# Kernel optimization log

Measured on AMD Instinct MI355X. Metric: run time of the kernel, lower is better.

## Reference

```python
import jax, jax.numpy as jnp
import numpy as np
from math import sqrt

D_MODEL, N_H, D_H, D_CQ, D_CKV, D_HR = 2048, 16, 128, 768, 512, 64
B, S = 1, 2048


def _rope_cos_sin(seq_len, dim, base=10000.0):
    inv_freq = 1.0 / (base ** (jnp.arange(0, dim, 2, dtype=jnp.float32) / dim))
    ang = jnp.arange(seq_len, dtype=jnp.float32)[:, None] * inv_freq[None, :]  # (S, dim//2)
    return jnp.cos(ang), jnp.sin(ang)


def _rope(t, cos, sin):
    # t: (B, S, ..., dim) with sequence on axis 1; interleaved complex pairs
    shp = t.shape
    d2 = shp[-1] // 2
    tr = t.reshape(shp[:-1] + (d2, 2))
    x0, x1 = tr[..., 0], tr[..., 1]
    bshape = (1, shp[1]) + (1,) * (x0.ndim - 3) + (d2,)
    cs, sn = cos.reshape(bshape), sin.reshape(bshape)
    return jnp.stack([x0 * cs - x1 * sn, x0 * sn + x1 * cs], axis=-1).reshape(shp)


def setup_inputs() -> dict:
    key = jax.random.key(0)
    ks = jax.random.split(key, 10)
    sc = 0.02
    inp = {
        "x": jax.random.normal(ks[0], (B, S, D_MODEL), jnp.float32),
        "mask": jnp.triu(jnp.ones((S, S), dtype=bool), k=1),  # True -> masked (causal)
        "w_norm": jnp.ones((D_MODEL,), jnp.float32),
        "w_cq": jax.random.normal(ks[1], (D_MODEL, D_CQ), jnp.float32) * sc,
        "w_q": jax.random.normal(ks[2], (D_CQ, N_H * D_H), jnp.float32) * sc,
        "w_qr": jax.random.normal(ks[3], (D_CQ, N_H * D_HR), jnp.float32) * sc,
        "w_ckv": jax.random.normal(ks[4], (D_MODEL, D_CKV), jnp.float32) * sc,
        "w_k": jax.random.normal(ks[5], (D_CKV, N_H * D_H), jnp.float32) * sc,
        "w_kr": jax.random.normal(ks[6], (D_MODEL, D_HR), jnp.float32) * sc,
        "w_v": jax.random.normal(ks[7], (D_CKV, D_MODEL), jnp.float32) * sc,
        "w_o": jax.random.normal(ks[8], (N_H * D_H, D_MODEL), jnp.float32) * sc,
    }
    return inp


def reference(x, mask, w_norm, w_cq, w_q, w_qr, w_ckv, w_k, w_kr, w_v, w_o):
    b, s, _ = x.shape
    eps = jnp.finfo(x.dtype).eps
    h = x * jax.lax.rsqrt(jnp.mean(x * x, axis=-1, keepdims=True) + eps) * w_norm  # RMSNorm
    cos, sin = _rope_cos_sin(s, D_HR)

    c_q = h @ w_cq  # (b, s, d_c_q)
    q_c = (c_q @ w_q).reshape(b, s, N_H, D_H).transpose(0, 2, 1, 3)          # (b, h, s, d_h)
    q_r = _rope((c_q @ w_qr).reshape(b, s, N_H, D_HR), cos, sin).transpose(0, 2, 1, 3)
    q = jnp.concatenate([q_c, q_r], axis=-1)  # (b, h, s, d_h + d_h_R)

    c_kv = h @ w_ckv  # (b, s, d_c_kv)
    k_c = (c_kv @ w_k).reshape(b, s, N_H, D_H).transpose(0, 2, 1, 3)
    k_r = _rope(h @ w_kr, cos, sin)[:, None]  # (b, 1, s, d_h_R), shared across heads
    k = jnp.concatenate([k_c, jnp.broadcast_to(k_r, (b, N_H, s, D_HR))], axis=-1)
    v = (c_kv @ w_v).reshape(b, s, N_H, D_H).transpose(0, 2, 1, 3)

    score = jnp.einsum('bhqd,bhkd->bhqk', q, k) / sqrt(D_H + D_HR)
    score = jnp.where(mask, -jnp.inf, score)
    attn = jax.nn.softmax(score, axis=-1)
    out = jnp.einsum('bhqk,bhkd->bhqd', attn, v)  # (b, h, s, d_h)
    out = out.transpose(0, 2, 1, 3).reshape(b, s, N_H * D_H) @ w_o
    return x + out
```

## Files before the change

kernel.cpp:

```cpp
#include <hip/hip_runtime.h>
#include <hip/hip_bf16.h>
#include <math.h>

#define D_MODEL 2048
#define N_H     16
#define D_H     128
#define D_CQ    768
#define D_CKV   512
#define D_HR    64
#define SEQ     2048
#define N_ACT1  1408
#define NSPLIT  4

typedef short bf16x8 __attribute__((ext_vector_type(8)));
typedef float f32x4  __attribute__((ext_vector_type(4)));

__device__ inline short f2bf(float f) {
  union { float f; unsigned u; } v; v.f = f;
  unsigned r = (v.u + 0x7fff + ((v.u >> 16) & 1)) >> 16;
  return (short)r;
}
__device__ inline float bf2f(short s) {
  union { float f; unsigned u; } v; v.u = ((unsigned)(unsigned short)s) << 16;
  return v.f;
}

__device__ inline void gld_lds16(const void* g, void* l) {
#if __has_builtin(__builtin_amdgcn_global_load_lds)
  __builtin_amdgcn_global_load_lds(
      (const __attribute__((address_space(1))) unsigned int*)g,
      (__attribute__((address_space(3))) unsigned int*)l, 16, 0, 0);
#else
  int lane = threadIdx.x & 63;
  *((uint4*)l + lane) = *(const uint4*)g;
#endif
}

struct CastJobs {
  const float* src[8];
  short* dst[8];
  int K[8];
  int pref[9];
  int nx[8];
};

__global__ __launch_bounds__(256) void prep_all(
    CastJobs J, const float* __restrict__ x, const float* __restrict__ wn,
    short* __restrict__ hb) {
  int bid = blockIdx.x;
  int tid = threadIdx.x;

  if (bid >= J.pref[8]) {
    int row = bid - J.pref[8];
    const float* xr = x + (size_t)row * D_MODEL;
    float ss = 0.f;
    for (int i = tid; i < D_MODEL; i += 256) { float v = xr[i]; ss += v * v; }
    __shared__ float red[256];
    red[tid] = ss;
    __syncthreads();
    for (int s = 128; s > 0; s >>= 1) {
      if (tid < s) red[tid] += red[tid + s];
      __syncthreads();
    }
    float scale = rsqrtf(red[0] / (float)D_MODEL + 1.1920929e-7f);
    short* hbr = hb + (size_t)row * D_MODEL;
    for (int i = tid; i < D_MODEL; i += 256) hbr[i] = f2bf(xr[i] * scale * wn[i]);
    return;
  }

  int j = 0;
#pragma unroll
  for (int t = 0; t < 8; t++)
    if (bid >= J.pref[t + 1]) j = t + 1;
  int lid = bid - J.pref[j];
  int nx = J.nx[j];
  int ty = lid / nx, tx = lid - ty * nx;
  int n0 = tx * 64, k0 = ty * 64;
  int K = J.K[j];
  const float* W = J.src[j];
  short* Wt = J.dst[j];
  int Nfull = nx * 64;

  __shared__ short T[64][68];
#pragma unroll
  for (int it = 0; it < 16; it++) {
    int idx = it * 256 + tid;
    int r = idx >> 6, c = idx & 63;
    T[c][r] = f2bf(W[(size_t)(k0 + r) * Nfull + n0 + c]);
  }
  __syncthreads();
#pragma unroll
  for (int it = 0; it < 16; it++) {
    int idx = it * 256 + tid;
    int r = idx >> 6, c = idx & 63;
    Wt[(size_t)(n0 + r) * K + k0 + c] = T[r][c];
  }
}

__device__ __forceinline__ void gemm64_body(
    const short* __restrict__ A, const short* __restrict__ Bt,
    float* __restrict__ Cf, short* __restrict__ Cb, short* __restrict__ Cb2,
    const float* __restrict__ addv, int M, int N, int K, int lda, int ldb,
    int mode, int bxx, int byy) {
  __shared__ short As[2 * 64 * 64];
  __shared__ short Bs[2 * 128 * 64];
  int tid = threadIdx.x;
  int w = tid >> 6, l = tid & 63;
  int lq = l >> 4, l16 = l & 15;
  int bm = byy * 64, bn = bxx * 128;
  int wr = w >> 1, wc = w & 1;
  int wm0 = wr * 32, wn0 = wc * 64;

  f32x4 acc[2][4];
#pragma unroll
  for (int i = 0; i < 2; i++)
#pragma unroll
    for (int j = 0; j < 4; j++) acc[i][j] = (f32x4)0.f;

  int rsub = (l >> 3);
  int csub = ((l & 7) ^ rsub) << 3;

  auto stage = [&](int buf, int k0) {
    short* Asb = As + buf * (64 * 64);
    short* Bsb = Bs + buf * (128 * 64);
#pragma unroll
    for (int i = 0; i < 2; i++) {
      int r0 = i * 32 + w * 8;
      gld_lds16(A + (size_t)(bm + r0 + rsub) * lda + k0 + csub, Asb + r0 * 64);
    }
#pragma unroll
    for (int i = 0; i < 4; i++) {
      int r0 = i * 32 + w * 8;
      gld_lds16(Bt + (size_t)(bn + r0 + rsub) * ldb + k0 + csub, Bsb + r0 * 64);
    }
  };

  stage(0, 0);
  int cur = 0;
  for (int k0 = 0; k0 < K; k0 += 64) {
    __syncthreads();
    if (k0 + 64 < K) stage(cur ^ 1, k0 + 64);
    const short* Asb = As + cur * (64 * 64);
    const short* Bsb = Bs + cur * (128 * 64);

#pragma unroll
    for (int ks = 0; ks < 2; ks++) {
      bf16x8 af[2], bfr[4];
      int sw = ((ks * 4 + lq) ^ (l16 & 7)) << 3;
#pragma unroll
      for (int mt = 0; mt < 2; mt++)
        af[mt] = *(const bf16x8*)&Asb[(wm0 + mt * 16 + l16) * 64 + sw];
#pragma unroll
      for (int nt = 0; nt < 4; nt++)
        bfr[nt] = *(const bf16x8*)&Bsb[(wn0 + nt * 16 + l16) * 64 + sw];
#pragma unroll
      for (int mt = 0; mt < 2; mt++)
#pragma unroll
        for (int nt = 0; nt < 4; nt++)
          acc[mt][nt] = __builtin_amdgcn_mfma_f32_16x16x32_bf16(af[mt], bfr[nt], acc[mt][nt], 0, 0, 0);
    }
    cur ^= 1;
  }

#pragma unroll
  for (int mt = 0; mt < 2; mt++)
#pragma unroll
    for (int i = 0; i < 4; i++) {
      int row = bm + wm0 + mt * 16 + lq * 4 + i;
#pragma unroll
      for (int nt = 0; nt < 4; nt++) {
        int col = bn + wn0 + nt * 16 + l16;
        float v = acc[mt][nt][i];
        if (mode == 0) {
          size_t off = (size_t)row * N + col;
          if (addv) v += addv[off];
          Cf[off] = v;
        } else if (mode == 1) {
          Cb[(size_t)row * N + col] = f2bf(v);
        } else if (mode == 3) {
          if (col < 2048) {
            Cb[((size_t)(col >> 7) * M + row) * 192 + (col & 127)] = f2bf(v);
          } else {
            int cc = col - 2048;
            int hh = cc >> 6, dd = cc & 63;
            float partner = __shfl_xor(v, 1);
            float inv = __expf(-((float)(dd & ~1) / 64.0f) * 9.210340372f);
            float ang = (float)row * inv;
            float c = __cosf(ang), s = __sinf(ang);
            float res = ((dd & 1) == 0) ? (v * c - partner * s)
                                        : (partner * s + v * c);
            Cb[((size_t)hh * M + row) * 192 + 128 + dd] = f2bf(res);
          }
        } else {
          if (col < 2048) {
            Cb[((size_t)(col >> 7) * M + row) * 192 + (col & 127)] = f2bf(v);
          } else {
            Cb2[(size_t)row * D_MODEL + (col - 2048)] = f2bf(v);
          }
        }
      }
    }
}

__global__ __launch_bounds__(256) void gemm_bf16_64(
    const short* __restrict__ A, const short* __restrict__ Bt,
    float* __restrict__ Cf, short* __restrict__ Cb, short* __restrict__ Cb2,
    const float* __restrict__ addv, int M, int N, int K, int lda, int ldb,
    int mode) {
  gemm64_body(A, Bt, Cf, Cb, Cb2, addv, M, N, K, lda, ldb, mode,
              blockIdx.x, blockIdx.y);
}

__global__ __launch_bounds__(256) void gemm_qkv(
    const short* __restrict__ act1, const short* __restrict__ WT2,
    const short* __restrict__ WT3, short* __restrict__ qb,
    short* __restrict__ kb, short* __restrict__ vb) {
  int bx = blockIdx.x;
  if (bx < 24) {
    gemm64_body(act1, WT2, nullptr, qb, nullptr, nullptr,
                SEQ, 3072, D_CQ, N_ACT1, D_CQ, 3, bx, blockIdx.y);
  } else {
    gemm64_body(act1 + 768, WT3, nullptr, kb, vb, nullptr,
                SEQ, 4096, D_CKV, N_ACT1, D_CKV, 4, bx - 24, blockIdx.y);
  }
}

__global__ __launch_bounds__(256) void gemm_fin_split(
    const short* __restrict__ A, const short* __restrict__ Bt,
    float* __restrict__ P) {
  int z = blockIdx.z;
  gemm64_body(A + z * 1024, Bt + z * 1024, P + (size_t)z * SEQ * D_MODEL,
              nullptr, nullptr, nullptr, SEQ, D_MODEL, 1024, D_MODEL, D_MODEL,
              0, blockIdx.x, blockIdx.y);
}

__global__ __launch_bounds__(256) void gemm_fin_merge(
    const float* __restrict__ P, const float* __restrict__ x,
    float* __restrict__ out) {
  size_t i = ((size_t)blockIdx.x * 256 + threadIdx.x) * 4;
  float4 a = *(const float4*)(P + i);
  float4 b = *(const float4*)(P + (size_t)SEQ * D_MODEL + i);
  float4 c = *(const float4*)(x + i);
  float4 o;
  o.x = a.x + b.x + c.x;
  o.y = a.y + b.y + c.y;
  o.z = a.z + b.z + c.z;
  o.w = a.w + b.w + c.w;
  *(float4*)(out + i) = o;
}

__global__ void rope_k_kernel(const short* __restrict__ act1, short* __restrict__ kb) {
  int idx = blockIdx.x * blockDim.x + threadIdx.x;
  if (idx >= SEQ * 32) return;
  int j = idx & 31;
  int s = idx >> 5;
  const short* p = act1 + (size_t)s * N_ACT1 + 1280 + 2 * j;
  float x0 = bf2f(p[0]), x1 = bf2f(p[1]);
  float inv = __expf(-((float)(2 * j) / 64.0f) * 9.210340372f);
  float ang = (float)s * inv;
  float c = __cosf(ang), sn = __sinf(ang);
  short b0 = f2bf(x0 * c - x1 * sn);
  short b1 = f2bf(x0 * sn + x1 * c);
#pragma unroll
  for (int hh = 0; hh < N_H; hh++) {
    short* k = kb + ((size_t)hh * SEQ + s) * 192 + 128 + 2 * j;
    k[0] = b0;
    k[1] = b1;
  }
}

__global__ __launch_bounds__(256) void cast_v_t(
    const short* __restrict__ vb, short* __restrict__ vt) {
  int s0 = blockIdx.x * 64;
  int h = blockIdx.y;
  __shared__ short T[128][72];
  int tid = threadIdx.x;
#pragma unroll
  for (int it = 0; it < 32; it++) {
    int c = it * 256 + tid;
    int r = c >> 7, d = c & 127;
    T[d][r] = vb[(size_t)(s0 + r) * D_MODEL + h * 128 + d];
  }
  __syncthreads();
#pragma unroll
  for (int it = 0; it < 32; it++) {
    int c = it * 256 + tid;
    int d = c >> 6, s = c & 63;
    vt[(size_t)(h * 128 + d) * SEQ + s0 + s] = T[d][s];
  }
}

#define TQ 128
#define TK 64

__global__ __launch_bounds__(256, 2) void attn_mfma(
    const short* __restrict__ qb, const short* __restrict__ kb,
    const short* __restrict__ vt, short* __restrict__ Opart,
    float* __restrict__ Lpart) {
  int bid = blockIdx.x;
  int h = bid & 15;
  int rest = bid >> 4;
  int qt = 15 - (rest / NSPLIT);
  int split = rest % NSPLIT;
  int q0 = qt * TQ;
  int nk = 2 * (qt + 1);
  int tid = threadIdx.x;
  int wave = tid >> 6, lane = tid & 63;
  int lq = lane >> 4, l16 = lane & 15;

  __shared__ short Ks[TK * 192];
  __shared__ short Vs[128 * 64];
  __shared__ short Ps[TQ * 64];

  bf16x8 qf[2][6];
  {
    const short* qp = qb + ((size_t)h * SEQ + q0 + wave * 32 + l16) * 192;
#pragma unroll
    for (int mt = 0; mt < 2; mt++)
#pragma unroll
      for (int ks = 0; ks < 6; ks++)
        qf[mt][ks] = *(const bf16x8*)(qp + (size_t)mt * 16 * 192 + ks * 32 + lq * 8);
  }

  bf16x8 ones;
#pragma unroll
  for (int i = 0; i < 8; i++) ones[i] = (short)0x3F80;

  f32x4 O[2][8];
  f32x4 Ol[2];
#pragma unroll
  for (int mt = 0; mt < 2; mt++) {
    Ol[mt] = (f32x4)0.f;
#pragma unroll
    for (int i = 0; i < 8; i++) O[mt][i] = (f32x4)0.f;
  }
  const float scale = 0.07216878364870323f;

  int goffK[6];
#pragma unroll
  for (int i = 0; i < 6; i++) {
    int s = i * 256 + tid;
    int r = s / 24;
    int c = s - r * 24;
    goffK[i] = r * 192 + ((c ^ (r & 7)) << 3);
  }
  int goffV[4];
  int vrow[4];
#pragma unroll
  for (int i = 0; i < 4; i++) {
    int s = i * 256 + tid;
    int d = s >> 3;
    int p = s & 7;
    vrow[i] = d;
    goffV[i] = (p ^ (d & 7)) << 3;
  }
  const short* kb_h = kb + (size_t)h * SEQ * 192;
  const short* vt_h = vt + (size_t)h * 128 * SEQ;

  auto stage_k = [&](int k0s) {
#pragma unroll
    for (int i = 0; i < 6; i++)
      gld_lds16(kb_h + (size_t)k0s * 192 + goffK[i],
                Ks + (size_t)(i * 256 + wave * 64) * 8);
  };
  auto stage_v = [&](int k0s) {
#pragma unroll
    for (int i = 0; i < 4; i++)
      gld_lds16(vt_h + (size_t)vrow[i] * SEQ + k0s + goffV[i],
                Vs + (size_t)(i * 256 + wave * 64) * 8);
  };

  if (split < nk) stage_k(split * TK);

  for (int t = split; t < nk; t += NSPLIT) {
    int k0 = t * TK;
    __syncthreads();

    stage_v(k0);

    f32x4 S[2][4];
#pragma unroll
    for (int mt = 0; mt < 2; mt++)
#pragma unroll
      for (int nt = 0; nt < 4; nt++) S[mt][nt] = (f32x4)0.f;
    __builtin_amdgcn_s_setprio(1);
#pragma unroll
    for (int ks = 0; ks < 6; ks++) {
#pragma unroll
      for (int nt = 0; nt < 4; nt++) {
        int row = nt * 16 + l16;
        bf16x8 b = *(const bf16x8*)&Ks[row * 192 +
                                       (((ks * 4 + lq) ^ (l16 & 7)) << 3)];
#pragma unroll
        for (int mt = 0; mt < 2; mt++)
          S[mt][nt] = __builtin_amdgcn_mfma_f32_16x16x32_bf16(qf[mt][ks], b, S[mt][nt], 0, 0, 0);
      }
    }
    __builtin_amdgcn_s_setprio(0);

#pragma unroll
    for (int mt = 0; mt < 2; mt++)
#pragma unroll
      for (int i = 0; i < 4; i++) {
        int pr = wave * 32 + mt * 16 + lq * 4 + i;
        int row = q0 + pr;
        bool may = (k0 + 63 > row);
#pragma unroll
        for (int nt = 0; nt < 4; nt++) {
          float p;
          if (may && (k0 + nt * 16 + l16 > row)) p = 0.f;
          else p = __expf(S[mt][nt][i] * scale);
          int j = nt * 16 + l16;
          Ps[pr * 64 + ((((j >> 3) ^ (pr & 7)) << 3) | (j & 7))] = f2bf(p);
        }
      }

    __syncthreads();

    if (t + NSPLIT < nk) stage_k((t + NSPLIT) * TK);

    __builtin_amdgcn_s_setprio(1);
#pragma unroll
    for (int kh = 0; kh < 2; kh++) {
      bf16x8 a[2];
#pragma unroll
      for (int mt = 0; mt < 2; mt++) {
        int prw = wave * 32 + mt * 16 + l16;
        a[mt] = *(const bf16x8*)&Ps[prw * 64 +
                                    (((kh * 4 + lq) ^ (l16 & 7)) << 3)];
        Ol[mt] = __builtin_amdgcn_mfma_f32_16x16x32_bf16(a[mt], ones, Ol[mt], 0, 0, 0);
      }
#pragma unroll
      for (int nt = 0; nt < 8; nt++) {
        int d = nt * 16 + l16;
        bf16x8 b = *(const bf16x8*)&Vs[d * 64 +
                                       (((kh * 4 + lq) ^ (d & 7)) << 3)];
#pragma unroll
        for (int mt = 0; mt < 2; mt++)
          O[mt][nt] = __builtin_amdgcn_mfma_f32_16x16x32_bf16(a[mt], b, O[mt][nt], 0, 0, 0);
      }
    }
    __builtin_amdgcn_s_setprio(0);
  }

#pragma unroll
  for (int mt = 0; mt < 2; mt++)
#pragma unroll
    for (int i = 0; i < 4; i++) {
      int row = q0 + wave * 32 + mt * 16 + lq * 4 + i;
      size_t base = ((size_t)(split * N_H + h) * SEQ + row);
      size_t obase = base * 128;
#pragma unroll
      for (int nt = 0; nt < 8; nt++)
        Opart[obase + nt * 16 + l16] = f2bf(O[mt][nt][i]);
      if (l16 == 0) Lpart[base] = Ol[mt][i];
    }
}

__global__ __launch_bounds__(256) void attn_merge(
    const short* __restrict__ Opart, const float* __restrict__ Lpart,
    short* __restrict__ aob) {
  int q0 = blockIdx.x * 16;
  int h = blockIdx.y;
  int tid = threadIdx.x;
#pragma unroll
  for (int i = 0; i < 8; i++) {
    int c = i * 256 + tid;
    int row = q0 + (c >> 7), d = c & 127;
    float denom = 0.f, num = 0.f;
#pragma unroll
    for (int p = 0; p < NSPLIT; p++) {
      size_t base = (size_t)(p * N_H + h) * SEQ + row;
      denom += Lpart[base];
      num += bf2f(Opart[base * 128 + d]);
    }
    aob[(size_t)row * D_MODEL + h * 128 + d] = f2bf(num / denom);
  }
}

extern "C" void kernel_launch(void* const* d_in, const int* in_sizes, int n_in,
                              void* d_out, int out_size, void* d_ws, size_t ws_size,
                              hipStream_t stream) {
  const float* x      = (const float*)d_in[0];
  const float* w_norm = (const float*)d_in[2];
  const float* w_cq   = (const float*)d_in[3];
  const float* w_q    = (const float*)d_in[4];
  const float* w_qr   = (const float*)d_in[5];
  const float* w_ckv  = (const float*)d_in[6];
  const float* w_k    = (const float*)d_in[7];
  const float* w_kr   = (const float*)d_in[8];
  const float* w_v    = (const float*)d_in[9];
  const float* w_o    = (const float*)d_in[10];
  float* out = (float*)d_out;

  char* ws = (char*)d_ws;
  short* h_bf  = (short*)ws;  ws += (size_t)SEQ * D_MODEL * 2;
  short* act1  = (short*)ws;  ws += (size_t)SEQ * N_ACT1 * 2;
  short* qb    = (short*)ws;  ws += (size_t)N_H * SEQ * 192 * 2;
  short* kb    = (short*)ws;  ws += (size_t)N_H * SEQ * 192 * 2;
  short* vb    = (short*)ws;  ws += (size_t)SEQ * D_MODEL * 2;
  short* vt    = (short*)ws;  ws += (size_t)SEQ * D_MODEL * 2;
  short* ao_bf = (short*)ws;  ws += (size_t)SEQ * D_MODEL * 2;
  short* Opart = (short*)ws;  ws += (size_t)NSPLIT * N_H * SEQ * 128 * 2;
  float* Lpart = (float*)ws;  ws += (size_t)NSPLIT * N_H * SEQ * 4;
  short* WT1   = (short*)ws;  ws += (size_t)N_ACT1 * D_MODEL * 2;
  short* WT2   = (short*)ws;  ws += (size_t)3072 * D_CQ * 2;
  short* WT3   = (short*)ws;  ws += (size_t)4096 * D_CKV * 2;
  short* WTO   = (short*)ws;  ws += (size_t)D_MODEL * D_MODEL * 2;

  float* Pfin = (float*)Opart;

  CastJobs J;
  J.src[0] = w_cq;  J.dst[0] = WT1;                              J.K[0] = D_MODEL; J.nx[0] = D_CQ / 64;
  J.src[1] = w_ckv; J.dst[1] = WT1 + (size_t)768 * D_MODEL;      J.K[1] = D_MODEL; J.nx[1] = D_CKV / 64;
  J.src[2] = w_kr;  J.dst[2] = WT1 + (size_t)1280 * D_MODEL;     J.K[2] = D_MODEL; J.nx[2] = D_HR / 64;
  J.src[3] = w_q;   J.dst[3] = WT2;                              J.K[3] = D_CQ;    J.nx[3] = 2048 / 64;
  J.src[4] = w_qr;  J.dst[4] = WT2 + (size_t)2048 * D_CQ;        J.K[4] = D_CQ;    J.nx[4] = 1024 / 64;
  J.src[5] = w_k;   J.dst[5] = WT3;                              J.K[5] = D_CKV;   J.nx[5] = 2048 / 64;
  J.src[6] = w_v;   J.dst[6] = WT3 + (size_t)2048 * D_CKV;       J.K[6] = D_CKV;   J.nx[6] = 2048 / 64;
  J.src[7] = w_o;   J.dst[7] = WTO;                              J.K[7] = D_MODEL; J.nx[7] = 2048 / 64;
  int pref = 0;
  for (int j = 0; j < 8; j++) {
    J.pref[j] = pref;
    pref += J.nx[j] * (J.K[j] / 64);
  }
  J.pref[8] = pref;
  prep_all<<<pref + SEQ, 256, 0, stream>>>(J, x, w_norm, h_bf);

  gemm_bf16_64<<<dim3(N_ACT1 / 128, SEQ / 64), 256, 0, stream>>>(
      h_bf, WT1, nullptr, act1, nullptr, nullptr, SEQ, N_ACT1, D_MODEL,
      D_MODEL, D_MODEL, 1);

  rope_k_kernel<<<(SEQ * 32 + 255) / 256, 256, 0, stream>>>(act1, kb);

  gemm_qkv<<<dim3(24 + 32, SEQ / 64), 256, 0, stream>>>(
      act1, WT2, WT3, qb, kb, vb);

  cast_v_t<<<dim3(SEQ / 64, N_H), 256, 0, stream>>>(vb, vt);

  attn_mfma<<<dim3((SEQ / TQ) * NSPLIT * N_H), 256, 0, stream>>>(qb, kb, vt, Opart, Lpart);
  attn_merge<<<dim3(SEQ / 16, N_H), 256, 0, stream>>>(Opart, Lpart, ao_bf);

  gemm_fin_split<<<dim3(D_MODEL / 128, SEQ / 64, 2), 256, 0, stream>>>(
      ao_bf, WTO, Pfin);
  gemm_fin_merge<<<(SEQ * D_MODEL) / (256 * 4), 256, 0, stream>>>(
      Pfin, x, out);
}
```

Measured before the change: 306.1 us.

## Fuse V transpose into QKV GEMM, double-buffer K, drop split-K output GEMM

The KV GEMM epilogue now writes V directly in transposed (d-major) layout with 4-wide stores, which removes the separate cast_v_t kernel and the vb buffer. The attention kernel double-buffers the K tile in LDS so the next K load is issued before the current tile's QK compute. The final output projection runs as a single GEMM that adds the residual in its epilogue, replacing the split-K GEMM and the merge kernel. The changes trade LDS footprint in attention (which may reduce occupancy) and fewer output-GEMM blocks for fewer launches and less global traffic.

```diff
diff --git a/kernel.cpp b/kernel.cpp
--- a/kernel.cpp
+++ b/kernel.cpp
@@ -13,6 +13,7 @@
 #define NSPLIT  4
 
 typedef short bf16x8 __attribute__((ext_vector_type(8)));
+typedef short short4v __attribute__((ext_vector_type(4)));
 typedef float f32x4  __attribute__((ext_vector_type(4)));
 
 __device__ inline short f2bf(float f) {
@@ -165,11 +166,20 @@
 #pragma unroll
   for (int mt = 0; mt < 2; mt++)
 #pragma unroll
-    for (int i = 0; i < 4; i++) {
-      int row = bm + wm0 + mt * 16 + lq * 4 + i;
-#pragma unroll
-      for (int nt = 0; nt < 4; nt++) {
-        int col = bn + wn0 + nt * 16 + l16;
+    for (int nt = 0; nt < 4; nt++) {
+      int col = bn + wn0 + nt * 16 + l16;
+      int row0 = bm + wm0 + mt * 16 + lq * 4;
+      if (mode == 4 && col >= 2048) {
+        int cc = col - 2048;
+        short4v v4;
+#pragma unroll
+        for (int i = 0; i < 4; i++) v4[i] = f2bf(acc[mt][nt][i]);
+        *(short4v*)&Cb2[(size_t)cc * SEQ + row0] = v4;
+        continue;
+      }
+#pragma unroll
+      for (int i = 0; i < 4; i++) {
+        int row = row0 + i;
         float v = acc[mt][nt][i];
         if (mode == 0) {
           size_t off = (size_t)row * N + col;
@@ -192,11 +202,7 @@
             Cb[((size_t)hh * M + row) * 192 + 128 + dd] = f2bf(res);
           }
         } else {
-          if (col < 2048) {
-            Cb[((size_t)(col >> 7) * M + row) * 192 + (col & 127)] = f2bf(v);
-          } else {
-            Cb2[(size_t)row * D_MODEL + (col - 2048)] = f2bf(v);
-          }
+          Cb[((size_t)(col >> 7) * M + row) * 192 + (col & 127)] = f2bf(v);
         }
       }
     }
@@ -214,39 +220,15 @@
 __global__ __launch_bounds__(256) void gemm_qkv(
     const short* __restrict__ act1, const short* __restrict__ WT2,
     const short* __restrict__ WT3, short* __restrict__ qb,
-    short* __restrict__ kb, short* __restrict__ vb) {
+    short* __restrict__ kb, short* __restrict__ vt) {
   int bx = blockIdx.x;
   if (bx < 24) {
     gemm64_body(act1, WT2, nullptr, qb, nullptr, nullptr,
                 SEQ, 3072, D_CQ, N_ACT1, D_CQ, 3, bx, blockIdx.y);
   } else {
-    gemm64_body(act1 + 768, WT3, nullptr, kb, vb, nullptr,
+    gemm64_body(act1 + 768, WT3, nullptr, kb, vt, nullptr,
                 SEQ, 4096, D_CKV, N_ACT1, D_CKV, 4, bx - 24, blockIdx.y);
   }
-}
-
-__global__ __launch_bounds__(256) void gemm_fin_split(
-    const short* __restrict__ A, const short* __restrict__ Bt,
-    float* __restrict__ P) {
-  int z = blockIdx.z;
-  gemm64_body(A + z * 1024, Bt + z * 1024, P + (size_t)z * SEQ * D_MODEL,
-              nullptr, nullptr, nullptr, SEQ, D_MODEL, 1024, D_MODEL, D_MODEL,
-              0, blockIdx.x, blockIdx.y);
-}
-
-__global__ __launch_bounds__(256) void gemm_fin_merge(
-    const float* __restrict__ P, const float* __restrict__ x,
-    float* __restrict__ out) {
-  size_t i = ((size_t)blockIdx.x * 256 + threadIdx.x) * 4;
-  float4 a = *(const float4*)(P + i);
-  float4 b = *(const float4*)(P + (size_t)SEQ * D_MODEL + i);
-  float4 c = *(const float4*)(x + i);
-  float4 o;
-  o.x = a.x + b.x + c.x;
-  o.y = a.y + b.y + c.y;
-  o.z = a.z + b.z + c.z;
-  o.w = a.w + b.w + c.w;
-  *(float4*)(out + i) = o;
 }
 
 __global__ void rope_k_kernel(const short* __restrict__ act1, short* __restrict__ kb) {
@@ -269,29 +251,9 @@
   }
 }
 
-__global__ __launch_bounds__(256) void cast_v_t(
-    const short* __restrict__ vb, short* __restrict__ vt) {
-  int s0 = blockIdx.x * 64;
-  int h = blockIdx.y;
-  __shared__ short T[128][72];
-  int tid = threadIdx.x;
-#pragma unroll
-  for (int it = 0; it < 32; it++) {
-    int c = it * 256 + tid;
-    int r = c >> 7, d = c & 127;
-    T[d][r] = vb[(size_t)(s0 + r) * D_MODEL + h * 128 + d];
-  }
-  __syncthreads();
-#pragma unroll
-  for (int it = 0; it < 32; it++) {
-    int c = it * 256 + tid;
-    int d = c >> 6, s = c & 63;
-    vt[(size_t)(h * 128 + d) * SEQ + s0 + s] = T[d][s];
-  }
-}
-
 #define TQ 128
 #define TK 64
+#define KSZ (TK * 192)
 
 __global__ __launch_bounds__(256, 2) void attn_mfma(
     const short* __restrict__ qb, const short* __restrict__ kb,
@@ -308,7 +270,7 @@
   int wave = tid >> 6, lane = tid & 63;
   int lq = lane >> 4, l16 = lane & 15;
 
-  __shared__ short Ks[TK * 192];
+  __shared__ short Ks[2 * KSZ];
   __shared__ short Vs[128 * 64];
   __shared__ short Ps[TQ * 64];
 
@@ -357,11 +319,11 @@
   const short* kb_h = kb + (size_t)h * SEQ * 192;
   const short* vt_h = vt + (size_t)h * 128 * SEQ;
 
-  auto stage_k = [&](int k0s) {
+  auto stage_k = [&](int k0s, int buf) {
 #pragma unroll
     for (int i = 0; i < 6; i++)
       gld_lds16(kb_h + (size_t)k0s * 192 + goffK[i],
-                Ks + (size_t)(i * 256 + wave * 64) * 8);
+                Ks + buf * KSZ + (size_t)(i * 256 + wave * 64) * 8);
   };
   auto stage_v = [&](int k0s) {
 #pragma unroll
@@ -370,14 +332,17 @@
                 Vs + (size_t)(i * 256 + wave * 64) * 8);
   };
 
-  if (split < nk) stage_k(split * TK);
+  if (split < nk) stage_k(split * TK, 0);
+  int kbuf = 0;
 
   for (int t = split; t < nk; t += NSPLIT) {
     int k0 = t * TK;
     __syncthreads();
 
     stage_v(k0);
-
+    if (t + NSPLIT < nk) stage_k((t + NSPLIT) * TK, kbuf ^ 1);
+
+    const short* Ksb = Ks + kbuf * KSZ;
     f32x4 S[2][4];
 #pragma unroll
     for (int mt = 0; mt < 2; mt++)
@@ -389,8 +354,8 @@
 #pragma unroll
       for (int nt = 0; nt < 4; nt++) {
         int row = nt * 16 + l16;
-        bf16x8 b = *(const bf16x8*)&Ks[row * 192 +
-                                       (((ks * 4 + lq) ^ (l16 & 7)) << 3)];
+        bf16x8 b = *(const bf16x8*)&Ksb[row * 192 +
+                                        (((ks * 4 + lq) ^ (l16 & 7)) << 3)];
 #pragma unroll
         for (int mt = 0; mt < 2; mt++)
           S[mt][nt] = __builtin_amdgcn_mfma_f32_16x16x32_bf16(qf[mt][ks], b, S[mt][nt], 0, 0, 0);
@@ -417,8 +382,6 @@
 
     __syncthreads();
 
-    if (t + NSPLIT < nk) stage_k((t + NSPLIT) * TK);
-
     __builtin_amdgcn_s_setprio(1);
 #pragma unroll
     for (int kh = 0; kh < 2; kh++) {
@@ -441,6 +404,7 @@
       }
     }
     __builtin_amdgcn_s_setprio(0);
+    kbuf ^= 1;
   }
 
 #pragma unroll
@@ -498,7 +462,6 @@
   short* act1  = (short*)ws;  ws += (size_t)SEQ * N_ACT1 * 2;
   short* qb    = (short*)ws;  ws += (size_t)N_H * SEQ * 192 * 2;
   short* kb    = (short*)ws;  ws += (size_t)N_H * SEQ * 192 * 2;
-  short* vb    = (short*)ws;  ws += (size_t)SEQ * D_MODEL * 2;
   short* vt    = (short*)ws;  ws += (size_t)SEQ * D_MODEL * 2;
   short* ao_bf = (short*)ws;  ws += (size_t)SEQ * D_MODEL * 2;
   short* Opart = (short*)ws;  ws += (size_t)NSPLIT * N_H * SEQ * 128 * 2;
@@ -507,8 +470,6 @@
   short* WT2   = (short*)ws;  ws += (size_t)3072 * D_CQ * 2;
   short* WT3   = (short*)ws;  ws += (size_t)4096 * D_CKV * 2;
   short* WTO   = (short*)ws;  ws += (size_t)D_MODEL * D_MODEL * 2;
-
-  float* Pfin = (float*)Opart;
 
   CastJobs J;
   J.src[0] = w_cq;  J.dst[0] = WT1;                              J.K[0] = D_MODEL; J.nx[0] = D_CQ / 64;
@@ -534,15 +495,12 @@
   rope_k_kernel<<<(SEQ * 32 + 255) / 256, 256, 0, stream>>>(act1, kb);
 
   gemm_qkv<<<dim3(24 + 32, SEQ / 64), 256, 0, stream>>>(
-      act1, WT2, WT3, qb, kb, vb);
-
-  cast_v_t<<<dim3(SEQ / 64, N_H), 256, 0, stream>>>(vb, vt);
+      act1, WT2, WT3, qb, kb, vt);
 
   attn_mfma<<<dim3((SEQ / TQ) * NSPLIT * N_H), 256, 0, stream>>>(qb, kb, vt, Opart, Lpart);
   attn_merge<<<dim3(SEQ / 16, N_H), 256, 0, stream>>>(Opart, Lpart, ao_bf);
 
-  gemm_fin_split<<<dim3(D_MODEL / 128, SEQ / 64, 2), 256, 0, stream>>>(
-      ao_bf, WTO, Pfin);
-  gemm_fin_merge<<<(SEQ * D_MODEL) / (256 * 4), 256, 0, stream>>>(
-      Pfin, x, out);
-}
+  gemm_bf16_64<<<dim3(D_MODEL / 128, SEQ / 64), 256, 0, stream>>>(
+      ao_bf, WTO, out, nullptr, nullptr, x, SEQ, D_MODEL, D_MODEL,
+      D_MODEL, D_MODEL, 0);
+}
```

New measurement: 281.9 us. -7.9%, faster.
